# Kernel optimization log

Hardware: AMD Instinct MI355X
Metric: run time of the kernel (lower is better)

The kernel has to match this reference:

```python
import jax, jax.numpy as jnp
import numpy as np

B, S, D, H = 2, 2048, 1024, 16
DK = D // H


def setup_inputs() -> dict:
    key = jax.random.key(0)
    ks = jax.random.split(key, 12)
    scale = 1.0 / np.sqrt(D)
    inp = {
        "query": jax.random.normal(ks[0], (B, S, D), jnp.float32),
        "key": jax.random.normal(ks[1], (B, S, D), jnp.float32),
        "value": jax.random.normal(ks[2], (B, S, D), jnp.float32),
        "mask": jnp.broadcast_to(jnp.tril(jnp.ones((S, S), bool)), (B, S, S)),
        "Wq": jax.random.normal(ks[3], (D, D), jnp.float32) * scale,
        "bq": jnp.zeros((D,), jnp.float32),
        "Wk": jax.random.normal(ks[4], (D, D), jnp.float32) * scale,
        "bk": jnp.zeros((D,), jnp.float32),
        "Wv": jax.random.normal(ks[5], (D, D), jnp.float32) * scale,
        "bv": jnp.zeros((D,), jnp.float32),
        "Wo": jax.random.normal(ks[6], (D, D), jnp.float32) * scale,
        "bo": jnp.zeros((D,), jnp.float32),
    }
    return inp


def _split_heads(x):
    # [B, S, D] -> [B, H, S, DK]
    return x.reshape(B, S, H, DK).transpose(0, 2, 1, 3)


def reference(query, key, value, mask, Wq, bq, Wk, bk, Wv, bv, Wo, bo):
    q = _split_heads(query @ Wq + bq)
    k = _split_heads(key @ Wk + bk)
    v = _split_heads(value @ Wv + bv)
    # scores: [B, H, S, S]
    scores = jnp.einsum("bhqd,bhkd->bhqk", q, k) / jnp.sqrt(jnp.float32(DK))
    scores = jnp.where(mask[:, None, :, :], scores, jnp.float32(-1e9))
    p_attn = jax.nn.softmax(scores, axis=-1)
    x = jnp.einsum("bhqk,bhkd->bhqd", p_attn, v)  # [B, H, S, DK]
    x = x.transpose(0, 2, 1, 3).reshape(B, S, D)
    return x @ Wo + bo
```

## Files before the change

kernel.cpp:

```cpp
#include <hip/hip_runtime.h>


#define S_LEN 2048
#define DMODEL 1024
#define NHEAD 16
#define DKH 64
#define QSCALE 0.18033688011112042f

typedef __attribute__((ext_vector_type(8))) short short8;
typedef __attribute__((ext_vector_type(4))) float f32x4;
typedef __attribute__((ext_vector_type(4))) unsigned short ushort4v;

__device__ __forceinline__ unsigned short f2bf(float f) {
  union { float f; unsigned int u; } v; v.f = f;
  unsigned int r = v.u + 0x7fffu + ((v.u >> 16) & 1u);
  return (unsigned short)(r >> 16);
}

__device__ __forceinline__ void gload_lds16(const void* g, void* l) {
  __builtin_amdgcn_global_load_lds(
      (const __attribute__((address_space(1))) void*)g,
      (__attribute__((address_space(3))) void*)l, 16, 0, 0);
}

__global__ __launch_bounds__(256) void transpose_cast(const float* __restrict__ W,
                                                      unsigned short* __restrict__ Wt) {
  __shared__ float tile[32][33];
  const int tx = threadIdx.x, ty = threadIdx.y;
  const int c0 = blockIdx.x * 32, r0 = blockIdx.y * 32;
#pragma unroll
  for (int i = 0; i < 32; i += 8)
    tile[ty + i][tx] = W[(r0 + ty + i) * 1024 + c0 + tx];
  __syncthreads();
#pragma unroll
  for (int i = 0; i < 32; i += 8)
    Wt[(c0 + ty + i) * 1024 + r0 + tx] = f2bf(tile[tx][ty + i]);
}

__global__ __launch_bounds__(256) void cast3(const float* __restrict__ s0,
                                             const float* __restrict__ s1,
                                             const float* __restrict__ s2,
                                             unsigned short* __restrict__ d0,
                                             unsigned short* __restrict__ d1,
                                             unsigned short* __restrict__ d2) {
  const int z = blockIdx.y;
  const float* src = (z == 0) ? s0 : (z == 1) ? s1 : s2;
  unsigned short* dst = (z == 0) ? d0 : (z == 1) ? d1 : d2;
  const int i = (blockIdx.x * 256 + threadIdx.x) * 8;
  float4 a = *(const float4*)&src[i];
  float4 b = *(const float4*)&src[i + 4];
  unsigned short u[8];
  u[0] = f2bf(a.x); u[1] = f2bf(a.y); u[2] = f2bf(a.z); u[3] = f2bf(a.w);
  u[4] = f2bf(b.x); u[5] = f2bf(b.y); u[6] = f2bf(b.z); u[7] = f2bf(b.w);
  *(short8*)&dst[i] = *(short8*)u;
}

__global__ __launch_bounds__(256) void qkv_gemm(
    const unsigned short* Qc, const unsigned short* Kc, const unsigned short* Vc,
    const unsigned short* WtQ, const unsigned short* WtK, const unsigned short* WtV,
    const float* bq, const float* bk, const float* bv,
    unsigned short* Qw, unsigned short* Kw, unsigned short* Vtw) {
  __shared__ unsigned short Alds[128 * 32];
  __shared__ unsigned short Blds[128 * 32];
  const int z = blockIdx.z;
  const unsigned short* A  = (z == 0) ? Qc : (z == 1) ? Kc : Vc;
  const unsigned short* Wt = (z == 0) ? WtQ : (z == 1) ? WtK : WtV;
  const float* bias        = (z == 0) ? bq : (z == 1) ? bk : bv;

  const int tid = threadIdx.x;
  const int m0 = blockIdx.y * 128, n0 = blockIdx.x * 128;
  const int wid = tid >> 6, lane = tid & 63;
  const int lg = lane >> 4, lr = lane & 15;
  const int wr = (wid >> 1) * 64, wc = (wid & 1) * 64;
  const int srow_base = wid * 32 + (lane >> 2);
  const int scol = (lane & 3) * 8;

  f32x4 acc[4][4] = {};

  for (int kt = 0; kt < 1024; kt += 32) {
#pragma unroll
    for (int i = 0; i < 2; i++) {
      const int row = srow_base + i * 16;
      char* ldst_a = (char*)Alds + wid * 2048 + i * 1024;
      char* ldst_b = (char*)Blds + wid * 2048 + i * 1024;
      gload_lds16(A  + (m0 + row) * 1024 + kt + scol, ldst_a);
      gload_lds16(Wt + (n0 + row) * 1024 + kt + scol, ldst_b);
    }
    __syncthreads();
    short8 af[4], bfr[4];
#pragma unroll
    for (int i = 0; i < 4; i++) af[i] = *(short8*)&Alds[(wr + i * 16 + lr) * 32 + lg * 8];
#pragma unroll
    for (int i = 0; i < 4; i++) bfr[i] = *(short8*)&Blds[(wc + i * 16 + lr) * 32 + lg * 8];
#pragma unroll
    for (int mi = 0; mi < 4; mi++)
#pragma unroll
      for (int ni = 0; ni < 4; ni++)
        acc[mi][ni] = __builtin_amdgcn_mfma_f32_16x16x32_bf16(af[mi], bfr[ni], acc[mi][ni], 0, 0, 0);
    __syncthreads();
  }

  if (z < 2) {
    unsigned short* O = (z == 0) ? Qw : Kw;
    const float sc = (z == 0) ? QSCALE : 1.0f;
#pragma unroll
    for (int mi = 0; mi < 4; mi++)
#pragma unroll
      for (int ni = 0; ni < 4; ni++) {
        const int gn = n0 + wc + ni * 16 + lr;
        const int h = gn >> 6, dk = gn & 63;
        const float bb = bias[gn];
#pragma unroll
        for (int r = 0; r < 4; r++) {
          const int gm = m0 + wr + mi * 16 + lg * 4 + r;
          const int b = gm >> 11, s = gm & 2047;
          O[(((b * NHEAD + h) * S_LEN + s) << 6) + dk] = f2bf((acc[mi][ni][r] + bb) * sc);
        }
      }
  } else {
#pragma unroll
    for (int mi = 0; mi < 4; mi++)
#pragma unroll
      for (int ni = 0; ni < 4; ni++) {
        const int gn = n0 + wc + ni * 16 + lr;
        const int h = gn >> 6, dk = gn & 63;
        const float bb = bias[gn];
        const int gm = m0 + wr + mi * 16 + lg * 4;
        const int b = gm >> 11, s = gm & 2047;
        unsigned short u[4];
#pragma unroll
        for (int r = 0; r < 4; r++) u[r] = f2bf(acc[mi][ni][r] + bb);
        *(ushort4v*)&Vtw[(((b * NHEAD + h) * DKH + dk) << 11) + s] = *(ushort4v*)u;
      }
  }
}

__global__ __launch_bounds__(256) void oproj_gemm(const unsigned short* __restrict__ A,
                                                  const unsigned short* __restrict__ Wt,
                                                  const float* __restrict__ bias,
                                                  float* __restrict__ Of32) {
  __shared__ unsigned short Alds[64 * 32];
  __shared__ unsigned short Blds[128 * 32];
  const int tid = threadIdx.x;
  const int m0 = blockIdx.y * 64, n0 = blockIdx.x * 128;
  const int wid = tid >> 6, lane = tid & 63;
  const int lg = lane >> 4, lr = lane & 15;
  const int wc = wid * 32;
  const int arow = wid * 16 + (lane >> 2);
  const int brow_base = wid * 32 + (lane >> 2);
  const int scol = (lane & 3) * 8;

  f32x4 acc[4][2] = {};

  for (int kt = 0; kt < 1024; kt += 32) {
    gload_lds16(A + (m0 + arow) * 1024 + kt + scol, (char*)Alds + wid * 1024);
#pragma unroll
    for (int i = 0; i < 2; i++) {
      const int row = brow_base + i * 16;
      gload_lds16(Wt + (n0 + row) * 1024 + kt + scol,
                  (char*)Blds + wid * 2048 + i * 1024);
    }
    __syncthreads();
    short8 af[4], bfr[2];
#pragma unroll
    for (int i = 0; i < 4; i++) af[i] = *(short8*)&Alds[(i * 16 + lr) * 32 + lg * 8];
#pragma unroll
    for (int j = 0; j < 2; j++) bfr[j] = *(short8*)&Blds[(wc + j * 16 + lr) * 32 + lg * 8];
#pragma unroll
    for (int mi = 0; mi < 4; mi++)
#pragma unroll
      for (int ni = 0; ni < 2; ni++)
        acc[mi][ni] = __builtin_amdgcn_mfma_f32_16x16x32_bf16(af[mi], bfr[ni], acc[mi][ni], 0, 0, 0);
    __syncthreads();
  }

#pragma unroll
  for (int mi = 0; mi < 4; mi++)
#pragma unroll
    for (int ni = 0; ni < 2; ni++) {
      const int gn = n0 + wc + ni * 16 + lr;
      const float bb = bias[gn];
#pragma unroll
      for (int r = 0; r < 4; r++) {
        const int gm = m0 + mi * 16 + lg * 4 + r;
        Of32[gm * 1024 + gn] = acc[mi][ni][r] + bb;
      }
    }
}

__global__ __launch_bounds__(256) void attn_k(const unsigned short* __restrict__ Q,
                                              const unsigned short* __restrict__ K,
                                              const unsigned short* __restrict__ Vt,
                                              unsigned short* __restrict__ X) {
  __shared__ unsigned short Kb[2][4096];
  __shared__ unsigned short Vb[2][4096];
  __shared__ unsigned short Plds[4][16][72];
  const int tid = threadIdx.x;
  const int wid = tid >> 6, lane = tid & 63;
  const int lg = lane >> 4, lr = lane & 15;
  const int bh = blockIdx.y;
  const unsigned short* Qh = Q + bh * (S_LEN * DKH);
  const char* KhB = (const char*)(K + bh * (S_LEN * DKH));
  const char* VtB = (const char*)(Vt + bh * (DKH * S_LEN));
  const int b = bh >> 4, h = bh & 15;

  const int srow_lo = (lane >> 3);
  const int scolb = (lane & 7) * 16;

  short8 ones8;
#pragma unroll
  for (int i = 0; i < 8; i++) ones8[i] = (short)0x3F80;

  for (int pass = 0; pass < 2; ++pass) {
    const int qt = (pass == 0) ? (int)blockIdx.x : 31 - (int)blockIdx.x;
    const int qr = qt * 64 + wid * 16;

    short8 qf[2];
#pragma unroll
    for (int c = 0; c < 2; c++) qf[c] = *(const short8*)&Qh[(qr + lr) * 64 + c * 32 + lg * 8];

    f32x4 o[4] = {};
    f32x4 lsv = {};

    int cur = 0;
    __syncthreads();

#define STAGE(BUF, KV)                                                          \
    {                                                                           \
      _Pragma("unroll")                                                         \
      for (int i = 0; i < 2; i++) {                                             \
        const int row = wid * 16 + i * 8 + srow_lo;                             \
        const int sw = scolb ^ ((row & 7) << 4);                                \
        gload_lds16(KhB + ((KV) + row) * 128 + sw,                              \
                    (char*)&Kb[BUF][0] + wid * 2048 + i * 1024);                \
        gload_lds16(VtB + row * 4096 + (KV) * 2 + sw,                           \
                    (char*)&Vb[BUF][0] + wid * 2048 + i * 1024);                \
      }                                                                         \
    }

    STAGE(cur, 0);

    for (int t = 0; t <= qt; ++t) {
      __syncthreads();
      if (t < qt) STAGE(cur ^ 1, (t + 1) * 64);
      const int kv = t * 64;
      const bool diag = (t == qt);

      f32x4 sa[4] = {};
#pragma unroll
      for (int jf = 0; jf < 4; jf++) {
        const int row = jf * 16 + lr;
#pragma unroll
        for (int c = 0; c < 2; c++) {
          const int cb = (c * 64 + lg * 16) ^ ((lr & 7) << 4);
          short8 kf = *(const short8*)((const char*)&Kb[cur][0] + row * 128 + cb);
          sa[jf] = __builtin_amdgcn_mfma_f32_16x16x32_bf16(qf[c], kf, sa[jf], 0, 0, 0);
        }
      }

#pragma unroll
      for (int jf = 0; jf < 4; jf++) {
        const int j = kv + jf * 16 + lr;
#pragma unroll
        for (int r = 0; r < 4; r++) {
          float s = sa[jf][r];
          if (diag) s = (j > qr + lg * 4 + r) ? -1e30f : s;
          Plds[wid][lg * 4 + r][jf * 16 + lr] = f2bf(exp2f(s));
        }
      }
      short8 pa[2];
#pragma unroll
      for (int c = 0; c < 2; c++) pa[c] = *(short8*)&Plds[wid][lr][c * 32 + lg * 8];
#pragma unroll
      for (int f = 0; f < 4; f++) {
        const int row = f * 16 + lr;
#pragma unroll
        for (int c = 0; c < 2; c++) {
          const int cb = (c * 64 + lg * 16) ^ ((lr & 7) << 4);
          short8 vf = *(const short8*)((const char*)&Vb[cur][0] + row * 128 + cb);
          o[f] = __builtin_amdgcn_mfma_f32_16x16x32_bf16(pa[c], vf, o[f], 0, 0, 0);
        }
      }
#pragma unroll
      for (int c = 0; c < 2; c++)
        lsv = __builtin_amdgcn_mfma_f32_16x16x32_bf16(pa[c], ones8, lsv, 0, 0, 0);
      cur ^= 1;
    }

#pragma unroll
    for (int r = 0; r < 4; r++) {
      const float inv = 1.f / lsv[r];
      const int q = qr + lg * 4 + r;
#pragma unroll
      for (int f = 0; f < 4; f++)
        X[(b * S_LEN + q) * DMODEL + h * DKH + f * 16 + lr] = f2bf(o[f][r] * inv);
    }
  }
#undef STAGE
}

extern "C" void kernel_launch(void* const* d_in, const int* in_sizes, int n_in,
                              void* d_out, int out_size, void* d_ws, size_t ws_size,
                              hipStream_t stream) {
  const float* query = (const float*)d_in[0];
  const float* key   = (const float*)d_in[1];
  const float* value = (const float*)d_in[2];
  const float* Wq = (const float*)d_in[4];
  const float* bq = (const float*)d_in[5];
  const float* Wk = (const float*)d_in[6];
  const float* bk = (const float*)d_in[7];
  const float* Wv = (const float*)d_in[8];
  const float* bv = (const float*)d_in[9];
  const float* Wo = (const float*)d_in[10];
  const float* bo = (const float*)d_in[11];
  float* out = (float*)d_out;

  unsigned short* ws = (unsigned short*)d_ws;
  unsigned short* WtQ = ws;
  unsigned short* WtK = ws + 1048576;
  unsigned short* WtV = ws + 2097152;
  unsigned short* WtO = ws + 3145728;
  unsigned short* Qw  = ws + 4194304;
  unsigned short* Kw  = ws + 8388608;
  unsigned short* Vtw = ws + 12582912;
  unsigned short* Xw  = ws + 16777216;
  unsigned short* Qc  = ws + 20971520;
  unsigned short* Kc  = ws + 25165824;
  unsigned short* Vc  = ws + 29360128;
  (void)in_sizes; (void)n_in; (void)out_size; (void)ws_size;

  dim3 tb(32, 8), tg(32, 32);
  transpose_cast<<<tg, tb, 0, stream>>>(Wq, WtQ);
  transpose_cast<<<tg, tb, 0, stream>>>(Wk, WtK);
  transpose_cast<<<tg, tb, 0, stream>>>(Wv, WtV);
  transpose_cast<<<tg, tb, 0, stream>>>(Wo, WtO);

  cast3<<<dim3(2048, 3), 256, 0, stream>>>(query, key, value, Qc, Kc, Vc);

  qkv_gemm<<<dim3(8, 32, 3), 256, 0, stream>>>(Qc, Kc, Vc, WtQ, WtK, WtV,
                                               bq, bk, bv, Qw, Kw, Vtw);

  attn_k<<<dim3(16, 32), 256, 0, stream>>>(Qw, Kw, Vtw, Xw);

  oproj_gemm<<<dim3(8, 64), 256, 0, stream>>>(Xw, WtO, bo, out);
}
```

Measured before the change: 149.4 us.

## Double-buffer GEMM LDS tiles, swap grid block order, add MFMA priority hints

Both the QKV and output-projection GEMMs now use two LDS buffers. The next K-tile is prefetched with global_load_lds while MFMAs run on the current tile, and one of the two barriers per iteration is removed. The grid mapping is swapped so consecutive blocks walk along M and share the same weight column tile, which may improve L2 reuse. The attention kernel raises wave priority around its MFMA sections so matrix work is issued ahead of other waves. Doubling LDS use may reduce occupancy.

```diff
diff --git a/kernel.cpp b/kernel.cpp
--- a/kernel.cpp
+++ b/kernel.cpp
@@ -60,15 +60,15 @@
     const unsigned short* WtQ, const unsigned short* WtK, const unsigned short* WtV,
     const float* bq, const float* bk, const float* bv,
     unsigned short* Qw, unsigned short* Kw, unsigned short* Vtw) {
-  __shared__ unsigned short Alds[128 * 32];
-  __shared__ unsigned short Blds[128 * 32];
+  __shared__ unsigned short Alds[2][4096];
+  __shared__ unsigned short Blds[2][4096];
   const int z = blockIdx.z;
   const unsigned short* A  = (z == 0) ? Qc : (z == 1) ? Kc : Vc;
   const unsigned short* Wt = (z == 0) ? WtQ : (z == 1) ? WtK : WtV;
   const float* bias        = (z == 0) ? bq : (z == 1) ? bk : bv;
 
   const int tid = threadIdx.x;
-  const int m0 = blockIdx.y * 128, n0 = blockIdx.x * 128;
+  const int m0 = blockIdx.x * 128, n0 = blockIdx.y * 128;
   const int wid = tid >> 6, lane = tid & 63;
   const int lg = lane >> 4, lr = lane & 15;
   const int wr = (wid >> 1) * 64, wc = (wid & 1) * 64;
@@ -77,28 +77,36 @@
 
   f32x4 acc[4][4] = {};
 
+#define GSTAGE(BUF, KT)                                                          \
+  {                                                                              \
+    _Pragma("unroll")                                                            \
+    for (int i = 0; i < 2; i++) {                                                \
+      const int row = srow_base + i * 16;                                        \
+      gload_lds16(A  + (m0 + row) * 1024 + (KT) + scol,                          \
+                  (char*)&Alds[BUF][0] + wid * 2048 + i * 1024);                 \
+      gload_lds16(Wt + (n0 + row) * 1024 + (KT) + scol,                          \
+                  (char*)&Blds[BUF][0] + wid * 2048 + i * 1024);                 \
+    }                                                                            \
+  }
+
+  GSTAGE(0, 0)
+  int cur = 0;
   for (int kt = 0; kt < 1024; kt += 32) {
-#pragma unroll
-    for (int i = 0; i < 2; i++) {
-      const int row = srow_base + i * 16;
-      char* ldst_a = (char*)Alds + wid * 2048 + i * 1024;
-      char* ldst_b = (char*)Blds + wid * 2048 + i * 1024;
-      gload_lds16(A  + (m0 + row) * 1024 + kt + scol, ldst_a);
-      gload_lds16(Wt + (n0 + row) * 1024 + kt + scol, ldst_b);
-    }
     __syncthreads();
+    if (kt + 32 < 1024) GSTAGE(cur ^ 1, kt + 32)
     short8 af[4], bfr[4];
 #pragma unroll
-    for (int i = 0; i < 4; i++) af[i] = *(short8*)&Alds[(wr + i * 16 + lr) * 32 + lg * 8];
-#pragma unroll
-    for (int i = 0; i < 4; i++) bfr[i] = *(short8*)&Blds[(wc + i * 16 + lr) * 32 + lg * 8];
+    for (int i = 0; i < 4; i++) af[i] = *(short8*)&Alds[cur][(wr + i * 16 + lr) * 32 + lg * 8];
+#pragma unroll
+    for (int i = 0; i < 4; i++) bfr[i] = *(short8*)&Blds[cur][(wc + i * 16 + lr) * 32 + lg * 8];
 #pragma unroll
     for (int mi = 0; mi < 4; mi++)
 #pragma unroll
       for (int ni = 0; ni < 4; ni++)
         acc[mi][ni] = __builtin_amdgcn_mfma_f32_16x16x32_bf16(af[mi], bfr[ni], acc[mi][ni], 0, 0, 0);
-    __syncthreads();
-  }
+    cur ^= 1;
+  }
+#undef GSTAGE
 
   if (z < 2) {
     unsigned short* O = (z == 0) ? Qw : Kw;
@@ -139,10 +147,10 @@
                                                   const unsigned short* __restrict__ Wt,
                                                   const float* __restrict__ bias,
                                                   float* __restrict__ Of32) {
-  __shared__ unsigned short Alds[64 * 32];
-  __shared__ unsigned short Blds[128 * 32];
+  __shared__ unsigned short Alds[2][2048];
+  __shared__ unsigned short Blds[2][4096];
   const int tid = threadIdx.x;
-  const int m0 = blockIdx.y * 64, n0 = blockIdx.x * 128;
+  const int m0 = blockIdx.x * 64, n0 = blockIdx.y * 128;
   const int wid = tid >> 6, lane = tid & 63;
   const int lg = lane >> 4, lr = lane & 15;
   const int wc = wid * 32;
@@ -152,27 +160,36 @@
 
   f32x4 acc[4][2] = {};
 
+#define OSTAGE(BUF, KT)                                                          \
+  {                                                                              \
+    gload_lds16(A + (m0 + arow) * 1024 + (KT) + scol,                            \
+                (char*)&Alds[BUF][0] + wid * 1024);                              \
+    _Pragma("unroll")                                                            \
+    for (int i = 0; i < 2; i++) {                                                \
+      const int row = brow_base + i * 16;                                        \
+      gload_lds16(Wt + (n0 + row) * 1024 + (KT) + scol,                          \
+                  (char*)&Blds[BUF][0] + wid * 2048 + i * 1024);                 \
+    }                                                                            \
+  }
+
+  OSTAGE(0, 0)
+  int cur = 0;
   for (int kt = 0; kt < 1024; kt += 32) {
-    gload_lds16(A + (m0 + arow) * 1024 + kt + scol, (char*)Alds + wid * 1024);
-#pragma unroll
-    for (int i = 0; i < 2; i++) {
-      const int row = brow_base + i * 16;
-      gload_lds16(Wt + (n0 + row) * 1024 + kt + scol,
-                  (char*)Blds + wid * 2048 + i * 1024);
-    }
     __syncthreads();
+    if (kt + 32 < 1024) OSTAGE(cur ^ 1, kt + 32)
     short8 af[4], bfr[2];
 #pragma unroll
-    for (int i = 0; i < 4; i++) af[i] = *(short8*)&Alds[(i * 16 + lr) * 32 + lg * 8];
-#pragma unroll
-    for (int j = 0; j < 2; j++) bfr[j] = *(short8*)&Blds[(wc + j * 16 + lr) * 32 + lg * 8];
+    for (int i = 0; i < 4; i++) af[i] = *(short8*)&Alds[cur][(i * 16 + lr) * 32 + lg * 8];
+#pragma unroll
+    for (int j = 0; j < 2; j++) bfr[j] = *(short8*)&Blds[cur][(wc + j * 16 + lr) * 32 + lg * 8];
 #pragma unroll
     for (int mi = 0; mi < 4; mi++)
 #pragma unroll
       for (int ni = 0; ni < 2; ni++)
         acc[mi][ni] = __builtin_amdgcn_mfma_f32_16x16x32_bf16(af[mi], bfr[ni], acc[mi][ni], 0, 0, 0);
-    __syncthreads();
-  }
+    cur ^= 1;
+  }
+#undef OSTAGE
 
 #pragma unroll
   for (int mi = 0; mi < 4; mi++)
@@ -247,6 +264,7 @@
       const bool diag = (t == qt);
 
       f32x4 sa[4] = {};
+      __builtin_amdgcn_s_setprio(1);
 #pragma unroll
       for (int jf = 0; jf < 4; jf++) {
         const int row = jf * 16 + lr;
@@ -257,6 +275,7 @@
           sa[jf] = __builtin_amdgcn_mfma_f32_16x16x32_bf16(qf[c], kf, sa[jf], 0, 0, 0);
         }
       }
+      __builtin_amdgcn_s_setprio(0);
 
 #pragma unroll
       for (int jf = 0; jf < 4; jf++) {
@@ -271,6 +290,7 @@
       short8 pa[2];
 #pragma unroll
       for (int c = 0; c < 2; c++) pa[c] = *(short8*)&Plds[wid][lr][c * 32 + lg * 8];
+      __builtin_amdgcn_s_setprio(1);
 #pragma unroll
       for (int f = 0; f < 4; f++) {
         const int row = f * 16 + lr;
@@ -284,6 +304,7 @@
 #pragma unroll
       for (int c = 0; c < 2; c++)
         lsv = __builtin_amdgcn_mfma_f32_16x16x32_bf16(pa[c], ones8, lsv, 0, 0, 0);
+      __builtin_amdgcn_s_setprio(0);
       cur ^= 1;
     }
 
@@ -337,10 +358,10 @@
 
   cast3<<<dim3(2048, 3), 256, 0, stream>>>(query, key, value, Qc, Kc, Vc);
 
-  qkv_gemm<<<dim3(8, 32, 3), 256, 0, stream>>>(Qc, Kc, Vc, WtQ, WtK, WtV,
+  qkv_gemm<<<dim3(32, 8, 3), 256, 0, stream>>>(Qc, Kc, Vc, WtQ, WtK, WtV,
                                                bq, bk, bv, Qw, Kw, Vtw);
 
   attn_k<<<dim3(16, 32), 256, 0, stream>>>(Qw, Kw, Vtw, Xw);
 
-  oproj_gemm<<<dim3(8, 64), 256, 0, stream>>>(Xw, WtO, bo, out);
-}
+  oproj_gemm<<<dim3(64, 8), 256, 0, stream>>>(Xw, WtO, bo, out);
+}
```

Result: faster. 141.9 us (-5.0%).
